# Optimization experiments

Measured on AMD Instinct MI355X. Metric: run time of the kernel, lower is better.

The kernel has to match this reference:

```python
import jax, jax.numpy as jnp
import numpy as np

H = 8        # num_heads
KNN = 16     # k nearest neighbors
D = 256      # input_dim
LN_EPS = 1e-5


def _make_params(key, D):
    ks = jax.random.split(key, 10)
    def lin(k, din, dout):
        k1, k2 = jax.random.split(k)
        lim = 1.0 / np.sqrt(din)
        W = jax.random.uniform(k1, (din, dout), jnp.float32, -lim, lim)
        b = jax.random.uniform(k2, (dout,), jnp.float32, -lim, lim)
        return W, b
    Wq, bq = lin(ks[0], D, D)
    Wk, bk = lin(ks[1], D, D)
    Wv, bv = lin(ks[2], D, D)
    Wo1, bo1 = lin(ks[3], D, D)
    ln_g = jnp.ones((D,), jnp.float32)
    ln_b = jnp.zeros((D,), jnp.float32)
    Wo2, bo2 = lin(ks[4], D, D)
    return dict(Wq=Wq, bq=bq, Wk=Wk, bk=bk, Wv=Wv, bv=bv,
                Wo1=Wo1, bo1=bo1, ln_g=ln_g, ln_b=ln_b, Wo2=Wo2, bo2=bo2)


def setup_inputs() -> dict:
    key = jax.random.key(0)
    k1, k2, k3, k4, k5 = jax.random.split(key, 5)
    B, N, M = 2, 2048, 4096
    inp = {
        "src": jax.random.normal(k1, (B, N, 3), jnp.float32),
        "tgt": jax.random.normal(k2, (B, M, 3), jnp.float32),
        "src_fea": jax.random.normal(k3, (B, N, D), jnp.float32),
        "tgt_fea": jax.random.normal(k4, (B, M, D), jnp.float32),
    }
    inp.update(_make_params(k5, D))
    return inp


def _cdist(x, y):
    # Euclidean distance [B,N,M], matching torch.cdist(p=2)
    x2 = jnp.sum(x * x, axis=-1, keepdims=True)          # [B,N,1]
    y2 = jnp.sum(y * y, axis=-1, keepdims=True)          # [B,M,1]
    sq = x2 + jnp.swapaxes(y2, -1, -2) - 2.0 * jnp.einsum('bnc,bmc->bnm', x, y)
    return jnp.sqrt(jnp.maximum(sq, 0.0))


def _layernorm(x, g, b):
    mu = jnp.mean(x, axis=-1, keepdims=True)
    var = jnp.mean((x - mu) ** 2, axis=-1, keepdims=True)
    return (x - mu) * jax.lax.rsqrt(var + LN_EPS) * g + b


def reference(src, tgt, src_fea, tgt_fea, Wq, bq, Wk, bk, Wv, bv,
              Wo1, bo1, ln_g, ln_b, Wo2, bo2):
    B, N, Dm = src_fea.shape
    M = tgt.shape[1]
    dk = Dm // H
    scale = dk ** (-0.5)

    # kNN mask: distances [B,N,M], topk smallest -> boolean mask
    dist = _cdist(src, tgt)
    _, knn_idx = jax.lax.top_k(-dist, KNN)               # [B,N,KNN]
    bi = jnp.arange(B)[:, None, None]
    ni = jnp.arange(N)[None, :, None]
    mask = jnp.zeros((B, N, M), bool).at[bi, ni, knn_idx].set(True)

    # projections -> [B,H,*,dk]
    Q = (src_fea @ Wq + bq).reshape(B, N, H, dk).transpose(0, 2, 1, 3)
    K = (tgt_fea @ Wk + bk).reshape(B, M, H, dk).transpose(0, 2, 1, 3)
    V = (tgt_fea @ Wv + bv).reshape(B, M, H, dk).transpose(0, 2, 1, 3)

    scores = jnp.einsum('bhnd,bhmd->bhnm', Q, K) * scale
    scores = jnp.where(mask[:, None], scores, -jnp.inf)
    attn = jax.nn.softmax(scores, axis=-1)               # [B,H,N,M]

    out = jnp.einsum('bhnm,bhmd->bhnd', attn, V)
    out = out.transpose(0, 2, 1, 3).reshape(B, N, Dm)

    x = out + src_fea
    h = jax.nn.relu(_layernorm(x @ Wo1 + bo1, ln_g, ln_b))
    updated = h @ Wo2 + bo2

    avg_attn = jnp.mean(attn, axis=1)                    # [B,N,M]
    return updated, avg_attn
```

## Files before the change

### kernel.cpp

```cpp
#include <hip/hip_runtime.h>
#include <math.h>

#define BB 2
#define NN 2048
#define MM 4096
#define DD 256
#define HH 8
#define DK 32
#define KNN 16

typedef __attribute__((ext_vector_type(8))) short short8;
typedef __attribute__((ext_vector_type(4))) short short4v;
typedef __attribute__((ext_vector_type(4))) float f32x4;
typedef unsigned long long u64;
typedef unsigned short u16;

static __device__ __forceinline__ u16 f2bf(float f) {
    union { float f; unsigned u; } v; v.f = f;
    unsigned r = v.u + 0x7FFF + ((v.u >> 16) & 1);
    return (u16)(r >> 16);
}
static __device__ __forceinline__ float bf2f(u16 u) {
    union { unsigned u; float f; } v; v.u = ((unsigned)u) << 16;
    return v.f;
}

__global__ __launch_bounds__(256)
void wtrans(const float* W0, const float* W1, const float* W2, const float* W3, const float* W4,
            u16* O0, u16* O1, u16* O2, u16* O3, u16* O4)
{
    __shared__ float tile[64][65];
    const int bid = blockIdx.x;
    const int m = bid >> 4, tl = bid & 15;
    const int tr = (tl >> 2) * 64, tc = (tl & 3) * 64;
    const float* W = m == 0 ? W0 : m == 1 ? W1 : m == 2 ? W2 : m == 3 ? W3 : W4;
    u16*        O = m == 0 ? O0 : m == 1 ? O1 : m == 2 ? O2 : m == 3 ? O3 : O4;
    const int c = threadIdx.x & 63, r4 = threadIdx.x >> 6;
    #pragma unroll
    for (int i = 0; i < 16; ++i) {
        const int r = (r4 << 4) + i;
        tile[r][c] = W[(size_t)(tr + r) * 256 + tc + c];
    }
    __syncthreads();
    #pragma unroll
    for (int i = 0; i < 16; ++i) {
        const int cc = (r4 << 4) + i;
        O[(size_t)(tc + cc) * 256 + tr + c] = f2bf(tile[c][cc]);
    }
}

static __device__ __forceinline__ void gemm64_body(
    const float* __restrict__ A, size_t row0, const u16* __restrict__ WT, int col0,
    u16* As, u16* Bs, int t, f32x4 acc[2][2])
{
    const int lane = t & 63, w = t >> 6;
    const int wr = (w >> 1) * 32, wc = (w & 1) * 32;
    for (int k0 = 0; k0 < 256; k0 += 64) {
        #pragma unroll
        for (int e = 0; e < 2; ++e) {
            const int flat = t + (e << 8);
            const int r = flat >> 3, kc = (flat & 7) << 3;
            const int off = ((r << 7) + (kc << 1)) ^ ((r & 7) << 4);
            const float* ap = A + (row0 + r) * 256 + k0 + kc;
            float4 a0 = *(const float4*)ap;
            float4 a1 = *(const float4*)(ap + 4);
            short8 s;
            s[0] = (short)f2bf(a0.x); s[1] = (short)f2bf(a0.y);
            s[2] = (short)f2bf(a0.z); s[3] = (short)f2bf(a0.w);
            s[4] = (short)f2bf(a1.x); s[5] = (short)f2bf(a1.y);
            s[6] = (short)f2bf(a1.z); s[7] = (short)f2bf(a1.w);
            *(short8*)((char*)As + off) = s;
            *(short8*)((char*)Bs + off) = *(const short8*)(WT + (size_t)(col0 + r) * 256 + k0 + kc);
        }
        __syncthreads();
        #pragma unroll
        for (int kk = 0; kk < 64; kk += 32) {
            const int kbo = (kk + ((lane >> 4) << 3)) << 1;
            short8 af[2], bfr[2];
            #pragma unroll
            for (int i = 0; i < 2; ++i) {
                const int ra = wr + (i << 4) + (lane & 15);
                af[i]  = *(const short8*)((const char*)As + (((ra << 7) + kbo) ^ ((ra & 7) << 4)));
                const int rb = wc + (i << 4) + (lane & 15);
                bfr[i] = *(const short8*)((const char*)Bs + (((rb << 7) + kbo) ^ ((rb & 7) << 4)));
            }
            #pragma unroll
            for (int mi = 0; mi < 2; ++mi)
                #pragma unroll
                for (int ni = 0; ni < 2; ++ni)
                    acc[mi][ni] = __builtin_amdgcn_mfma_f32_16x16x32_bf16(af[mi], bfr[ni], acc[mi][ni], 0, 0, 0);
        }
        __syncthreads();
    }
}

__global__ __launch_bounds__(256, 4)
void mega_kernel(const float* __restrict__ src, const float* __restrict__ tgt,
                 int* __restrict__ knn_idx,
                 const float* __restrict__ tgt_fea, const float* __restrict__ src_fea,
                 const u16* __restrict__ WTq, const u16* __restrict__ WTkv,
                 const float* __restrict__ bq, const float* __restrict__ bk,
                 const float* __restrict__ bv,
                 float* __restrict__ Qb, u16* __restrict__ Kbf, u16* __restrict__ Vbf,
                 float* __restrict__ avg)
{
    __shared__ u16 As[64 * 64];
    __shared__ u16 Bs[64 * 64];
    const int bid = blockIdx.x;
    const int t = threadIdx.x;
    const int lane = t & 63;
    const int lid = bid / 11;
    const int role = bid % 11;

    if (role < 4) {
        const int kb = lid * 4 + role;
        const int bn = (kb << 2) + (t >> 6);
        const int b = bn >> 11;
        const float* sp = src + (size_t)bn * 3;
        const float px = sp[0], py = sp[1], pz = sp[2];
        const float x2 = px * px + py * py + pz * pz;
        const float* tb = tgt + (size_t)b * MM * 3;
        unsigned key[64];
        #pragma unroll
        for (int j = 0; j < 64; ++j) {
            const int m = (j << 6) + lane;
            const float tx = tb[m * 3 + 0], ty = tb[m * 3 + 1], tz = tb[m * 3 + 2];
            const float y2 = tx * tx + ty * ty + tz * tz;
            const float dt = px * tx + py * ty + pz * tz;
            float d = (x2 + y2) - 2.0f * dt;
            d = d > 0.f ? d : 0.f;
            const unsigned q20 = (unsigned)fminf(d * 32768.0f, 1048575.0f);
            key[j] = (q20 << 12) | (unsigned)m;
        }
        unsigned last1 = 0;
        unsigned mykey = 0xFFFFFFFFu;
        for (int sel = 0; sel < 20; ++sel) {
            unsigned c0 = ~0u, c1 = ~0u, c2 = ~0u, c3 = ~0u;
            #pragma unroll
            for (int j = 0; j < 64; j += 4) {
                const unsigned u0 = key[j + 0] - last1; c0 = u0 < c0 ? u0 : c0;
                const unsigned u1 = key[j + 1] - last1; c1 = u1 < c1 ? u1 : c1;
                const unsigned u2 = key[j + 2] - last1; c2 = u2 < c2 ? u2 : c2;
                const unsigned u3 = key[j + 3] - last1; c3 = u3 < c3 ? u3 : c3;
            }
            unsigned best = c0 < c1 ? c0 : c1;
            const unsigned bst2 = c2 < c3 ? c2 : c3;
            best = best < bst2 ? best : bst2;
            #pragma unroll
            for (int s = 32; s; s >>= 1) {
                const unsigned o = __shfl_xor(best, s, 64);
                best = o < best ? o : best;
            }
            const unsigned winner = best + last1;
            if (lane == sel) mykey = winner;
            last1 = winner + 1;
        }
        const int midx = (int)(mykey & 0xFFFu);
        u64 ex = ~0ULL;
        if (lane < 20) {
            const float* tp = tb + (size_t)midx * 3;
            const double pxd = px, pyd = py, pzd = pz;
            const double tx = tp[0], ty = tp[1], tz = tp[2];
            const double x2d = pxd * pxd + pyd * pyd + pzd * pzd;
            const double y2d = tx * tx + ty * ty + tz * tz;
            const double dtd = pxd * tx + pyd * ty + pzd * tz;
            double dd = (x2d + y2d) - 2.0 * dtd;
            dd = dd > 0.0 ? dd : 0.0;
            ex = (((u64)__double_as_longlong(dd)) & ~0xFFFULL) | (u64)midx;
        }
        int rank = 0;
        #pragma unroll
        for (int i = 0; i < 20; ++i) {
            const u64 o = __shfl(ex, i, 64);
            rank += (o < ex) ? 1 : 0;
        }
        if (lane < 20 && rank < 16)
            knn_idx[(size_t)bn * KNN + rank] = midx;
        return;
    }

    if (role < 8) {
        const int kvb = lid * 4 + (role - 4);
        const size_t row0 = (size_t)(kvb >> 3) * 64;
        const int col0 = (kvb & 7) * 64;
        f32x4 acc[2][2] = {};
        gemm64_body(tgt_fea, row0, WTkv, col0, As, Bs, t, acc);
        const int w = t >> 6;
        const int wr = (w >> 1) * 32, wc = (w & 1) * 32;
        const bool isv = col0 >= 256;
        u16* ob = isv ? Vbf : Kbf;
        const float* bs = isv ? bv : bk;
        const int cb = (isv ? col0 - 256 : col0) + wc;
        const int cq = lane & 15, rq = (lane >> 4) << 2;
        #pragma unroll
        for (int ni = 0; ni < 2; ++ni) {
            const int c = cb + (ni << 4) + cq;
            const float bval = bs[c];
            #pragma unroll
            for (int mi = 0; mi < 2; ++mi) {
                const size_t r = row0 + wr + (mi << 4) + rq;
                #pragma unroll
                for (int e = 0; e < 4; ++e)
                    ob[(r + e) * 256 + c] = f2bf(acc[mi][ni][e] + bval);
            }
        }
        return;
    }

    if (role == 8) {
        const int qb = lid;
        const size_t row0 = (size_t)(qb >> 2) * 64;
        const int col0 = (qb & 3) * 64;
        f32x4 acc[2][2] = {};
        gemm64_body(src_fea, row0, WTq, col0, As, Bs, t, acc);
        const int w = t >> 6;
        const int wr = (w >> 1) * 32, wc = (w & 1) * 32;
        const int cq = lane & 15, rq = (lane >> 4) << 2;
        #pragma unroll
        for (int ni = 0; ni < 2; ++ni) {
            const int c = col0 + wc + (ni << 4) + cq;
            const float bval = bq[c];
            #pragma unroll
            for (int mi = 0; mi < 2; ++mi) {
                const size_t rbase = (row0 + wr + (mi << 4) + rq) * 256 + c;
                #pragma unroll
                for (int e = 0; e < 4; ++e)
                    Qb[rbase + (size_t)e * 256] = acc[mi][ni][e] + bval;
            }
        }
        return;
    }

    {
        const int zb = lid * 2 + (role - 9);
        f32x4 z = {0.f, 0.f, 0.f, 0.f};
        f32x4* pz = (f32x4*)avg;
        const int base = zb * 256 + t;
        #pragma unroll
        for (int i = 0; i < 32; ++i)
            pz[base + i * 131072] = z;
    }
}

__global__ __launch_bounds__(256)
void attn_kernel(const float* __restrict__ Q, const u16* __restrict__ Kb,
                 const u16* __restrict__ Vb, const int* __restrict__ knn_idx,
                 const float* __restrict__ src_fea,
                 u16* __restrict__ Xb, float* __restrict__ avg_attn)
{
    __shared__ float q_sh[4][256];
    __shared__ float pw_sh[4][8][17];
    __shared__ int   idx_sh[4][16];
    const int t = threadIdx.x;
    const int wid = t >> 6, lane = t & 63;
    const int bn = (blockIdx.x << 2) + wid;
    const int b = bn >> 11;
    const int h = lane >> 3, k2 = lane & 7;

    *(float4*)&q_sh[wid][lane << 2] = *(const float4*)(Q + (size_t)bn * 256 + (lane << 2));
    const int ia = knn_idx[(size_t)bn * KNN + k2];
    const int ib = knn_idx[(size_t)bn * KNN + 8 + k2];
    __syncthreads();

    const u16* Ka = Kb + ((size_t)b * MM + ia) * 256 + h * DK;
    const u16* Kc = Kb + ((size_t)b * MM + ib) * 256 + h * DK;
    const float* qh = &q_sh[wid][h * DK];
    float s0 = 0.f, s1 = 0.f;
    #pragma unroll
    for (int j = 0; j < DK; j += 8) {
        const short8 ka = *(const short8*)(Ka + j);
        const short8 kc = *(const short8*)(Kc + j);
        #pragma unroll
        for (int e = 0; e < 8; ++e) {
            const float qv = qh[j + e];
            s0 = fmaf(qv, bf2f((u16)ka[e]), s0);
            s1 = fmaf(qv, bf2f((u16)kc[e]), s1);
        }
    }
    s0 *= 0.17677669529663688f;
    s1 *= 0.17677669529663688f;

    float m = fmaxf(s0, s1);
    m = fmaxf(m, __shfl_xor(m, 1, 64));
    m = fmaxf(m, __shfl_xor(m, 2, 64));
    m = fmaxf(m, __shfl_xor(m, 4, 64));
    const float e0 = expf(s0 - m), e1 = expf(s1 - m);
    float sum = e0 + e1;
    sum += __shfl_xor(sum, 1, 64);
    sum += __shfl_xor(sum, 2, 64);
    sum += __shfl_xor(sum, 4, 64);
    const float inv = 1.0f / sum;
    const float p0 = e0 * inv, p1 = e1 * inv;

    float a0 = p0, a1 = p1;
    a0 += __shfl_xor(a0, 8, 64);  a1 += __shfl_xor(a1, 8, 64);
    a0 += __shfl_xor(a0, 16, 64); a1 += __shfl_xor(a1, 16, 64);
    a0 += __shfl_xor(a0, 32, 64); a1 += __shfl_xor(a1, 32, 64);
    if (h == 0) {
        avg_attn[(size_t)bn * MM + ia] = a0 * 0.125f;
        avg_attn[(size_t)bn * MM + ib] = a1 * 0.125f;
        idx_sh[wid][k2] = ia;
        idx_sh[wid][8 + k2] = ib;
    }
    pw_sh[wid][h][k2] = p0;
    pw_sh[wid][h][8 + k2] = p1;
    __syncthreads();

    const int d0 = lane << 2;
    const int h2 = lane >> 3;
    float o0 = 0.f, o1 = 0.f, o2 = 0.f, o3 = 0.f;
    #pragma unroll
    for (int k = 0; k < KNN; ++k) {
        const float p = pw_sh[wid][h2][k];
        const int ik = idx_sh[wid][k];
        const short4v v4 = *(const short4v*)(Vb + ((size_t)b * MM + ik) * 256 + d0);
        o0 = fmaf(p, bf2f((u16)v4[0]), o0);
        o1 = fmaf(p, bf2f((u16)v4[1]), o1);
        o2 = fmaf(p, bf2f((u16)v4[2]), o2);
        o3 = fmaf(p, bf2f((u16)v4[3]), o3);
    }
    const float4 sf = *(const float4*)(src_fea + (size_t)bn * 256 + d0);
    short4v xo;
    xo[0] = (short)f2bf(o0 + sf.x);
    xo[1] = (short)f2bf(o1 + sf.y);
    xo[2] = (short)f2bf(o2 + sf.z);
    xo[3] = (short)f2bf(o3 + sf.w);
    *(short4v*)(Xb + (size_t)bn * 256 + d0) = xo;
}

__global__ __launch_bounds__(256)
void gemm_wo1_ln(const u16* __restrict__ A, const u16* __restrict__ WT,
                 const float* __restrict__ bias,
                 const float* __restrict__ g, const float* __restrict__ bvec,
                 u16* __restrict__ outb)
{
    __shared__ u16 As[32 * 64];
    __shared__ u16 Bs[256 * 64];
    const int t = threadIdx.x, lane = t & 63, w = t >> 6;
    const size_t row0 = (size_t)blockIdx.x * 32;
    f32x4 acc[2][4] = {};
    for (int k0 = 0; k0 < 256; k0 += 64) {
        {
            const int r = t >> 3, kc = (t & 7) << 3;
            const int off = ((r << 7) + (kc << 1)) ^ ((r & 7) << 4);
            *(short8*)((char*)As + off) = *(const short8*)(A + (row0 + r) * 256 + k0 + kc);
        }
        #pragma unroll
        for (int e = 0; e < 8; ++e) {
            const int u = t + (e << 8);
            const int r = u >> 3, kc = (u & 7) << 3;
            const int off = ((r << 7) + (kc << 1)) ^ ((r & 7) << 4);
            *(short8*)((char*)Bs + off) = *(const short8*)(WT + (size_t)r * 256 + k0 + kc);
        }
        __syncthreads();
        #pragma unroll
        for (int kk = 0; kk < 64; kk += 32) {
            const int kbo = (kk + ((lane >> 4) << 3)) << 1;
            short8 af[2], bfr[4];
            #pragma unroll
            for (int i = 0; i < 2; ++i) {
                const int ra = (i << 4) + (lane & 15);
                af[i] = *(const short8*)((const char*)As + (((ra << 7) + kbo) ^ ((ra & 7) << 4)));
            }
            #pragma unroll
            for (int i = 0; i < 4; ++i) {
                const int rb = (w << 6) + (i << 4) + (lane & 15);
                bfr[i] = *(const short8*)((const char*)Bs + (((rb << 7) + kbo) ^ ((rb & 7) << 4)));
            }
            #pragma unroll
            for (int mi = 0; mi < 2; ++mi)
                #pragma unroll
                for (int ni = 0; ni < 4; ++ni)
                    acc[mi][ni] = __builtin_amdgcn_mfma_f32_16x16x32_bf16(af[mi], bfr[ni], acc[mi][ni], 0, 0, 0);
        }
        __syncthreads();
    }
    const int cq = lane & 15, rq = (lane >> 4) << 2;
    #pragma unroll
    for (int ni = 0; ni < 4; ++ni) {
        const float bval = bias[(w << 6) + (ni << 4) + cq];
        #pragma unroll
        for (int mi = 0; mi < 2; ++mi)
            #pragma unroll
            for (int e = 0; e < 4; ++e)
                acc[mi][ni][e] += bval;
    }
    float* ws1 = (float*)As;
    float* ws2 = ws1 + 128;
    #pragma unroll
    for (int mi = 0; mi < 2; ++mi)
        #pragma unroll
        for (int e = 0; e < 4; ++e) {
            float s1 = 0.f, s2 = 0.f;
            #pragma unroll
            for (int ni = 0; ni < 4; ++ni) { const float y = acc[mi][ni][e]; s1 += y; s2 += y * y; }
            s1 += __shfl_xor(s1, 1, 64); s2 += __shfl_xor(s2, 1, 64);
            s1 += __shfl_xor(s1, 2, 64); s2 += __shfl_xor(s2, 2, 64);
            s1 += __shfl_xor(s1, 4, 64); s2 += __shfl_xor(s2, 4, 64);
            s1 += __shfl_xor(s1, 8, 64); s2 += __shfl_xor(s2, 8, 64);
            if (cq == 0) {
                const int r = (mi << 4) + rq + e;
                ws1[(w << 5) + r] = s1;
                ws2[(w << 5) + r] = s2;
            }
        }
    __syncthreads();
    float g4[4], b4[4];
    #pragma unroll
    for (int ni = 0; ni < 4; ++ni) {
        const int c = (w << 6) + (ni << 4) + cq;
        g4[ni] = g[c]; b4[ni] = bvec[c];
    }
    #pragma unroll
    for (int mi = 0; mi < 2; ++mi)
        #pragma unroll
        for (int e = 0; e < 4; ++e) {
            const int r = (mi << 4) + rq + e;
            const float s1 = ws1[r] + ws1[32 + r] + ws1[64 + r] + ws1[96 + r];
            const float s2 = ws2[r] + ws2[32 + r] + ws2[64 + r] + ws2[96 + r];
            const float mean = s1 * (1.0f / 256.0f);
            const float var = s2 * (1.0f / 256.0f) - mean * mean;
            const float rstd = 1.0f / sqrtf(var + 1e-5f);
            #pragma unroll
            for (int ni = 0; ni < 4; ++ni) {
                const int c = (w << 6) + (ni << 4) + cq;
                const float y = (acc[mi][ni][e] - mean) * rstd * g4[ni] + b4[ni];
                outb[(row0 + r) * 256 + c] = f2bf(fmaxf(y, 0.0f));
            }
        }
}

__global__ __launch_bounds__(256)
void gemm_wo2(const u16* __restrict__ A, const u16* __restrict__ WT,
              const float* __restrict__ bias, float* __restrict__ outf)
{
    __shared__ u16 As[32 * 64];
    __shared__ u16 Bs[128 * 64];
    const int t = threadIdx.x, lane = t & 63, w = t >> 6;
    const size_t row0 = (size_t)(blockIdx.x >> 1) * 32;
    const int col0 = (blockIdx.x & 1) * 128;
    f32x4 acc[2][2] = {};
    for (int k0 = 0; k0 < 256; k0 += 64) {
        {
            const int r = t >> 3, kc = (t & 7) << 3;
            const int off = ((r << 7) + (kc << 1)) ^ ((r & 7) << 4);
            *(short8*)((char*)As + off) = *(const short8*)(A + (row0 + r) * 256 + k0 + kc);
        }
        #pragma unroll
        for (int e = 0; e < 4; ++e) {
            const int u = t + (e << 8);
            const int r = u >> 3, kc = (u & 7) << 3;
            const int off = ((r << 7) + (kc << 1)) ^ ((r & 7) << 4);
            *(short8*)((char*)Bs + off) = *(const short8*)(WT + (size_t)(col0 + r) * 256 + k0 + kc);
        }
        __syncthreads();
        #pragma unroll
        for (int kk = 0; kk < 64; kk += 32) {
            const int kbo = (kk + ((lane >> 4) << 3)) << 1;
            short8 af[2], bfr[2];
            #pragma unroll
            for (int i = 0; i < 2; ++i) {
                const int ra = (i << 4) + (lane & 15);
                af[i] = *(const short8*)((const char*)As + (((ra << 7) + kbo) ^ ((ra & 7) << 4)));
                const int rb = (w << 5) + (i << 4) + (lane & 15);
                bfr[i] = *(const short8*)((const char*)Bs + (((rb << 7) + kbo) ^ ((rb & 7) << 4)));
            }
            #pragma unroll
            for (int mi = 0; mi < 2; ++mi)
                #pragma unroll
                for (int ni = 0; ni < 2; ++ni)
                    acc[mi][ni] = __builtin_amdgcn_mfma_f32_16x16x32_bf16(af[mi], bfr[ni], acc[mi][ni], 0, 0, 0);
        }
        __syncthreads();
    }
    const int cq = lane & 15, rq = (lane >> 4) << 2;
    #pragma unroll
    for (int ni = 0; ni < 2; ++ni) {
        const int c = col0 + (w << 5) + (ni << 4) + cq;
        const float bval = bias[c];
        #pragma unroll
        for (int mi = 0; mi < 2; ++mi) {
            const size_t rbase = (row0 + (mi << 4) + rq) * 256 + c;
            #pragma unroll
            for (int e = 0; e < 4; ++e)
                outf[rbase + (size_t)e * 256] = acc[mi][ni][e] + bval;
        }
    }
}

extern "C" void kernel_launch(void* const* d_in, const int* in_sizes, int n_in,
                              void* d_out, int out_size, void* d_ws, size_t ws_size,
                              hipStream_t stream) {
    const float* src     = (const float*)d_in[0];
    const float* tgt     = (const float*)d_in[1];
    const float* src_fea = (const float*)d_in[2];
    const float* tgt_fea = (const float*)d_in[3];
    const float* Wq  = (const float*)d_in[4];   const float* bq  = (const float*)d_in[5];
    const float* Wk  = (const float*)d_in[6];   const float* bk  = (const float*)d_in[7];
    const float* Wv  = (const float*)d_in[8];   const float* bv  = (const float*)d_in[9];
    const float* Wo1 = (const float*)d_in[10];  const float* bo1 = (const float*)d_in[11];
    const float* lng = (const float*)d_in[12];  const float* lnb = (const float*)d_in[13];
    const float* Wo2 = (const float*)d_in[14];  const float* bo2 = (const float*)d_in[15];
    (void)in_sizes; (void)n_in; (void)out_size; (void)ws_size;

    float* out     = (float*)d_out;
    float* updated = out;
    float* avg     = out + (size_t)BB * NN * DD;

    char* p = (char*)d_ws;
    u16* WTq  = (u16*)p;   p += 256 * 256 * 2;
    u16* WTk  = (u16*)p;   p += 256 * 256 * 2;
    u16* WTv  = (u16*)p;   p += 256 * 256 * 2;
    u16* WTo1 = (u16*)p;   p += 256 * 256 * 2;
    u16* WTo2 = (u16*)p;   p += 256 * 256 * 2;
    float* Qb = (float*)p; p += (size_t)BB * NN * DD * 4;
    u16* Kbf  = (u16*)p;   p += (size_t)BB * MM * DD * 2;
    u16* Vbf  = (u16*)p;   p += (size_t)BB * MM * DD * 2;
    int* knn  = (int*)p;   p += (size_t)BB * NN * KNN * 4;
    u16* Xbf  = (u16*)p;   p += (size_t)BB * NN * DD * 2;
    u16* Hbf  = (u16*)p;   p += (size_t)BB * NN * DD * 2;

    dim3 blk(256);
    wtrans<<<80, blk, 0, stream>>>(Wq, Wk, Wv, Wo1, Wo2, WTq, WTk, WTv, WTo1, WTo2);
    mega_kernel<<<2816, blk, 0, stream>>>(src, tgt, knn, tgt_fea, src_fea, WTq, WTk,
                                          bq, bk, bv, Qb, Kbf, Vbf, avg);
    attn_kernel<<<BB * NN / 4, blk, 0, stream>>>(Qb, Kbf, Vbf, knn, src_fea, Xbf, avg);
    gemm_wo1_ln<<<BB * NN / 32, blk, 0, stream>>>(Xbf, WTo1, bo1, lng, lnb, Hbf);
    gemm_wo2<<<BB * NN / 16, blk, 0, stream>>>(Hbf, WTo2, bo2, updated);
}
```

Before: 183.7 us.

## Fuse attention, Wo1+LayerNorm and Wo2 GEMMs into a single tail kernel

Replaces the separate attention, Wo1+LN and Wo2 kernels with one kernel per 4 query rows. It keeps the attention output and the LN/ReLU activations in shared memory, padded to a 16-row MFMA tile with zero rows. This removes two launches and the global round trips of the intermediate X and H buffers. In exchange, only 4 of the 16 MFMA rows are useful, and every block streams both full weight matrices directly from global/L2 with no LDS staging. That greatly raises total weight-read traffic.

```diff
diff --git a/kernel.cpp b/kernel.cpp
--- a/kernel.cpp
+++ b/kernel.cpp
@@ -147,8 +147,8 @@
             const unsigned bst2 = c2 < c3 ? c2 : c3;
             best = best < bst2 ? best : bst2;
             #pragma unroll
-            for (int s = 32; s; s >>= 1) {
-                const unsigned o = __shfl_xor(best, s, 64);
+            for (int s2 = 32; s2; s2 >>= 1) {
+                const unsigned o = __shfl_xor(best, s2, 64);
                 best = o < best ? o : best;
             }
             const unsigned winner = best + last1;
@@ -243,28 +243,44 @@
 }
 
 __global__ __launch_bounds__(256)
-void attn_kernel(const float* __restrict__ Q, const u16* __restrict__ Kb,
+void tail_kernel(const float* __restrict__ Q, const u16* __restrict__ Kb,
                  const u16* __restrict__ Vb, const int* __restrict__ knn_idx,
                  const float* __restrict__ src_fea,
-                 u16* __restrict__ Xb, float* __restrict__ avg_attn)
+                 const u16* __restrict__ WTo1, const float* __restrict__ bo1,
+                 const float* __restrict__ lng, const float* __restrict__ lnb,
+                 const u16* __restrict__ WTo2, const float* __restrict__ bo2,
+                 float* __restrict__ updated, float* __restrict__ avg_attn)
 {
     __shared__ float q_sh[4][256];
     __shared__ float pw_sh[4][8][17];
     __shared__ int   idx_sh[4][16];
+    __shared__ u16   Xs[16 * 256];
+    __shared__ u16   Hs[16 * 256];
+    __shared__ float2 red2[4][4];
     const int t = threadIdx.x;
-    const int wid = t >> 6, lane = t & 63;
-    const int bn = (blockIdx.x << 2) + wid;
+    const int w = t >> 6, lane = t & 63;
+    const int r0 = blockIdx.x << 2;
+    const int bn = r0 + w;
     const int b = bn >> 11;
     const int h = lane >> 3, k2 = lane & 7;
 
-    *(float4*)&q_sh[wid][lane << 2] = *(const float4*)(Q + (size_t)bn * 256 + (lane << 2));
+    {
+        unsigned* xz = (unsigned*)Xs;
+        unsigned* hz = (unsigned*)Hs;
+        #pragma unroll
+        for (int i = 0; i < 6; ++i) {
+            xz[512 + t + i * 256] = 0u;
+            hz[512 + t + i * 256] = 0u;
+        }
+    }
+
+    *(float4*)&q_sh[w][lane << 2] = *(const float4*)(Q + (size_t)bn * 256 + (lane << 2));
     const int ia = knn_idx[(size_t)bn * KNN + k2];
     const int ib = knn_idx[(size_t)bn * KNN + 8 + k2];
-    __syncthreads();
 
     const u16* Ka = Kb + ((size_t)b * MM + ia) * 256 + h * DK;
     const u16* Kc = Kb + ((size_t)b * MM + ib) * 256 + h * DK;
-    const float* qh = &q_sh[wid][h * DK];
+    const float* qh = &q_sh[w][h * DK];
     float s0 = 0.f, s1 = 0.f;
     #pragma unroll
     for (int j = 0; j < DK; j += 8) {
@@ -280,11 +296,11 @@
     s0 *= 0.17677669529663688f;
     s1 *= 0.17677669529663688f;
 
-    float m = fmaxf(s0, s1);
-    m = fmaxf(m, __shfl_xor(m, 1, 64));
-    m = fmaxf(m, __shfl_xor(m, 2, 64));
-    m = fmaxf(m, __shfl_xor(m, 4, 64));
-    const float e0 = expf(s0 - m), e1 = expf(s1 - m);
+    float mx = fmaxf(s0, s1);
+    mx = fmaxf(mx, __shfl_xor(mx, 1, 64));
+    mx = fmaxf(mx, __shfl_xor(mx, 2, 64));
+    mx = fmaxf(mx, __shfl_xor(mx, 4, 64));
+    const float e0 = expf(s0 - mx), e1 = expf(s1 - mx);
     float sum = e0 + e1;
     sum += __shfl_xor(sum, 1, 64);
     sum += __shfl_xor(sum, 2, 64);
@@ -299,191 +315,117 @@
     if (h == 0) {
         avg_attn[(size_t)bn * MM + ia] = a0 * 0.125f;
         avg_attn[(size_t)bn * MM + ib] = a1 * 0.125f;
-        idx_sh[wid][k2] = ia;
-        idx_sh[wid][8 + k2] = ib;
-    }
-    pw_sh[wid][h][k2] = p0;
-    pw_sh[wid][h][8 + k2] = p1;
+        idx_sh[w][k2] = ia;
+        idx_sh[w][8 + k2] = ib;
+    }
+    pw_sh[w][h][k2] = p0;
+    pw_sh[w][h][8 + k2] = p1;
+
+    {
+        const int d0 = lane << 2;
+        const int h2 = lane >> 3;
+        float o0 = 0.f, o1 = 0.f, o2 = 0.f, o3 = 0.f;
+        #pragma unroll
+        for (int k = 0; k < KNN; ++k) {
+            const float p = pw_sh[w][h2][k];
+            const int ik = idx_sh[w][k];
+            const short4v v4 = *(const short4v*)(Vb + ((size_t)b * MM + ik) * 256 + d0);
+            o0 = fmaf(p, bf2f((u16)v4[0]), o0);
+            o1 = fmaf(p, bf2f((u16)v4[1]), o1);
+            o2 = fmaf(p, bf2f((u16)v4[2]), o2);
+            o3 = fmaf(p, bf2f((u16)v4[3]), o3);
+        }
+        const float4 sf = *(const float4*)(src_fea + (size_t)bn * 256 + d0);
+        short4v xo;
+        xo[0] = (short)f2bf(o0 + sf.x);
+        xo[1] = (short)f2bf(o1 + sf.y);
+        xo[2] = (short)f2bf(o2 + sf.z);
+        xo[3] = (short)f2bf(o3 + sf.w);
+        const int off = ((w << 9) + (d0 << 1)) ^ ((w & 7) << 4);
+        *(short4v*)((char*)Xs + off) = xo;
+    }
     __syncthreads();
 
-    const int d0 = lane << 2;
-    const int h2 = lane >> 3;
-    float o0 = 0.f, o1 = 0.f, o2 = 0.f, o3 = 0.f;
+    const int cq = lane & 15, ks = lane >> 4;
+    f32x4 acc1[4] = {};
     #pragma unroll
-    for (int k = 0; k < KNN; ++k) {
-        const float p = pw_sh[wid][h2][k];
-        const int ik = idx_sh[wid][k];
-        const short4v v4 = *(const short4v*)(Vb + ((size_t)b * MM + ik) * 256 + d0);
-        o0 = fmaf(p, bf2f((u16)v4[0]), o0);
-        o1 = fmaf(p, bf2f((u16)v4[1]), o1);
-        o2 = fmaf(p, bf2f((u16)v4[2]), o2);
-        o3 = fmaf(p, bf2f((u16)v4[3]), o3);
-    }
-    const float4 sf = *(const float4*)(src_fea + (size_t)bn * 256 + d0);
-    short4v xo;
-    xo[0] = (short)f2bf(o0 + sf.x);
-    xo[1] = (short)f2bf(o1 + sf.y);
-    xo[2] = (short)f2bf(o2 + sf.z);
-    xo[3] = (short)f2bf(o3 + sf.w);
-    *(short4v*)(Xb + (size_t)bn * 256 + d0) = xo;
-}
-
-__global__ __launch_bounds__(256)
-void gemm_wo1_ln(const u16* __restrict__ A, const u16* __restrict__ WT,
-                 const float* __restrict__ bias,
-                 const float* __restrict__ g, const float* __restrict__ bvec,
-                 u16* __restrict__ outb)
-{
-    __shared__ u16 As[32 * 64];
-    __shared__ u16 Bs[256 * 64];
-    const int t = threadIdx.x, lane = t & 63, w = t >> 6;
-    const size_t row0 = (size_t)blockIdx.x * 32;
-    f32x4 acc[2][4] = {};
-    for (int k0 = 0; k0 < 256; k0 += 64) {
-        {
-            const int r = t >> 3, kc = (t & 7) << 3;
-            const int off = ((r << 7) + (kc << 1)) ^ ((r & 7) << 4);
-            *(short8*)((char*)As + off) = *(const short8*)(A + (row0 + r) * 256 + k0 + kc);
-        }
-        #pragma unroll
-        for (int e = 0; e < 8; ++e) {
-            const int u = t + (e << 8);
-            const int r = u >> 3, kc = (u & 7) << 3;
-            const int off = ((r << 7) + (kc << 1)) ^ ((r & 7) << 4);
-            *(short8*)((char*)Bs + off) = *(const short8*)(WT + (size_t)r * 256 + k0 + kc);
-        }
-        __syncthreads();
-        #pragma unroll
-        for (int kk = 0; kk < 64; kk += 32) {
-            const int kbo = (kk + ((lane >> 4) << 3)) << 1;
-            short8 af[2], bfr[4];
-            #pragma unroll
-            for (int i = 0; i < 2; ++i) {
-                const int ra = (i << 4) + (lane & 15);
-                af[i] = *(const short8*)((const char*)As + (((ra << 7) + kbo) ^ ((ra & 7) << 4)));
-            }
-            #pragma unroll
-            for (int i = 0; i < 4; ++i) {
-                const int rb = (w << 6) + (i << 4) + (lane & 15);
-                bfr[i] = *(const short8*)((const char*)Bs + (((rb << 7) + kbo) ^ ((rb & 7) << 4)));
-            }
-            #pragma unroll
-            for (int mi = 0; mi < 2; ++mi)
-                #pragma unroll
-                for (int ni = 0; ni < 4; ++ni)
-                    acc[mi][ni] = __builtin_amdgcn_mfma_f32_16x16x32_bf16(af[mi], bfr[ni], acc[mi][ni], 0, 0, 0);
-        }
-        __syncthreads();
-    }
-    const int cq = lane & 15, rq = (lane >> 4) << 2;
+    for (int s = 0; s < 4; ++s) {
+        const int colB = (w << 6) + (s << 4) + cq;
+        const u16* bp = WTo1 + (size_t)colB * 256;
+        #pragma unroll
+        for (int kk = 0; kk < 256; kk += 32) {
+            const int k8 = kk + (ks << 3);
+            const short8 af = *(const short8*)((const char*)Xs + (((cq << 9) + (k8 << 1)) ^ ((cq & 7) << 4)));
+            const short8 bfrg = *(const short8*)(bp + k8);
+            acc1[s] = __builtin_amdgcn_mfma_f32_16x16x32_bf16(af, bfrg, acc1[s], 0, 0, 0);
+        }
+        const float bval = bo1[colB];
+        #pragma unroll
+        for (int e = 0; e < 4; ++e) acc1[s][e] += bval;
+    }
+    {
+        #pragma unroll
+        for (int e = 0; e < 4; ++e) {
+            float v = acc1[0][e] + acc1[1][e] + acc1[2][e] + acc1[3][e];
+            float vv = acc1[0][e]*acc1[0][e] + acc1[1][e]*acc1[1][e]
+                     + acc1[2][e]*acc1[2][e] + acc1[3][e]*acc1[3][e];
+            v += __shfl_xor(v, 1, 64); vv += __shfl_xor(vv, 1, 64);
+            v += __shfl_xor(v, 2, 64); vv += __shfl_xor(vv, 2, 64);
+            v += __shfl_xor(v, 4, 64); vv += __shfl_xor(vv, 4, 64);
+            v += __shfl_xor(v, 8, 64); vv += __shfl_xor(vv, 8, 64);
+            if (ks == 0 && cq == 0) {
+                float2 pr; pr.x = v; pr.y = vv;
+                red2[w][e] = pr;
+            }
+        }
+    }
+    __syncthreads();
+    if (ks == 0) {
+        float g4[4], b4[4];
+        #pragma unroll
+        for (int s = 0; s < 4; ++s) {
+            const int colB = (w << 6) + (s << 4) + cq;
+            g4[s] = lng[colB]; b4[s] = lnb[colB];
+        }
+        #pragma unroll
+        for (int e = 0; e < 4; ++e) {
+            float S1 = 0.f, S2 = 0.f;
+            #pragma unroll
+            for (int w2 = 0; w2 < 4; ++w2) {
+                const float2 pr = red2[w2][e];
+                S1 += pr.x; S2 += pr.y;
+            }
+            const float mean = S1 * (1.0f / 256.0f);
+            const float var = S2 * (1.0f / 256.0f) - mean * mean;
+            const float rstd = 1.0f / sqrtf(var + 1e-5f);
+            #pragma unroll
+            for (int s = 0; s < 4; ++s) {
+                const int colB = (w << 6) + (s << 4) + cq;
+                const float y = (acc1[s][e] - mean) * rstd * g4[s] + b4[s];
+                const int off = ((e << 9) + (colB << 1)) ^ ((e & 7) << 4);
+                *(u16*)((char*)Hs + off) = f2bf(fmaxf(y, 0.0f));
+            }
+        }
+    }
+    __syncthreads();
+
     #pragma unroll
-    for (int ni = 0; ni < 4; ++ni) {
-        const float bval = bias[(w << 6) + (ni << 4) + cq];
-        #pragma unroll
-        for (int mi = 0; mi < 2; ++mi)
+    for (int s = 0; s < 4; ++s) {
+        const int colB = (w << 6) + (s << 4) + cq;
+        const u16* bp = WTo2 + (size_t)colB * 256;
+        f32x4 acc2 = {};
+        #pragma unroll
+        for (int kk = 0; kk < 256; kk += 32) {
+            const int k8 = kk + (ks << 3);
+            const short8 af = *(const short8*)((const char*)Hs + (((cq << 9) + (k8 << 1)) ^ ((cq & 7) << 4)));
+            const short8 bfrg = *(const short8*)(bp + k8);
+            acc2 = __builtin_amdgcn_mfma_f32_16x16x32_bf16(af, bfrg, acc2, 0, 0, 0);
+        }
+        if (ks == 0) {
+            const float bval = bo2[colB];
             #pragma unroll
             for (int e = 0; e < 4; ++e)
-                acc[mi][ni][e] += bval;
-    }
-    float* ws1 = (float*)As;
-    float* ws2 = ws1 + 128;
-    #pragma unroll
-    for (int mi = 0; mi < 2; ++mi)
-        #pragma unroll
-        for (int e = 0; e < 4; ++e) {
-            float s1 = 0.f, s2 = 0.f;
-            #pragma unroll
-            for (int ni = 0; ni < 4; ++ni) { const float y = acc[mi][ni][e]; s1 += y; s2 += y * y; }
-            s1 += __shfl_xor(s1, 1, 64); s2 += __shfl_xor(s2, 1, 64);
-            s1 += __shfl_xor(s1, 2, 64); s2 += __shfl_xor(s2, 2, 64);
-            s1 += __shfl_xor(s1, 4, 64); s2 += __shfl_xor(s2, 4, 64);
-            s1 += __shfl_xor(s1, 8, 64); s2 += __shfl_xor(s2, 8, 64);
-            if (cq == 0) {
-                const int r = (mi << 4) + rq + e;
-                ws1[(w << 5) + r] = s1;
-                ws2[(w << 5) + r] = s2;
-            }
-        }
-    __syncthreads();
-    float g4[4], b4[4];
-    #pragma unroll
-    for (int ni = 0; ni < 4; ++ni) {
-        const int c = (w << 6) + (ni << 4) + cq;
-        g4[ni] = g[c]; b4[ni] = bvec[c];
-    }
-    #pragma unroll
-    for (int mi = 0; mi < 2; ++mi)
-        #pragma unroll
-        for (int e = 0; e < 4; ++e) {
-            const int r = (mi << 4) + rq + e;
-            const float s1 = ws1[r] + ws1[32 + r] + ws1[64 + r] + ws1[96 + r];
-            const float s2 = ws2[r] + ws2[32 + r] + ws2[64 + r] + ws2[96 + r];
-            const float mean = s1 * (1.0f / 256.0f);
-            const float var = s2 * (1.0f / 256.0f) - mean * mean;
-            const float rstd = 1.0f / sqrtf(var + 1e-5f);
-            #pragma unroll
-            for (int ni = 0; ni < 4; ++ni) {
-                const int c = (w << 6) + (ni << 4) + cq;
-                const float y = (acc[mi][ni][e] - mean) * rstd * g4[ni] + b4[ni];
-                outb[(row0 + r) * 256 + c] = f2bf(fmaxf(y, 0.0f));
-            }
-        }
-}
-
-__global__ __launch_bounds__(256)
-void gemm_wo2(const u16* __restrict__ A, const u16* __restrict__ WT,
-              const float* __restrict__ bias, float* __restrict__ outf)
-{
-    __shared__ u16 As[32 * 64];
-    __shared__ u16 Bs[128 * 64];
-    const int t = threadIdx.x, lane = t & 63, w = t >> 6;
-    const size_t row0 = (size_t)(blockIdx.x >> 1) * 32;
-    const int col0 = (blockIdx.x & 1) * 128;
-    f32x4 acc[2][2] = {};
-    for (int k0 = 0; k0 < 256; k0 += 64) {
-        {
-            const int r = t >> 3, kc = (t & 7) << 3;
-            const int off = ((r << 7) + (kc << 1)) ^ ((r & 7) << 4);
-            *(short8*)((char*)As + off) = *(const short8*)(A + (row0 + r) * 256 + k0 + kc);
-        }
-        #pragma unroll
-        for (int e = 0; e < 4; ++e) {
-            const int u = t + (e << 8);
-            const int r = u >> 3, kc = (u & 7) << 3;
-            const int off = ((r << 7) + (kc << 1)) ^ ((r & 7) << 4);
-            *(short8*)((char*)Bs + off) = *(const short8*)(WT + (size_t)(col0 + r) * 256 + k0 + kc);
-        }
-        __syncthreads();
-        #pragma unroll
-        for (int kk = 0; kk < 64; kk += 32) {
-            const int kbo = (kk + ((lane >> 4) << 3)) << 1;
-            short8 af[2], bfr[2];
-            #pragma unroll
-            for (int i = 0; i < 2; ++i) {
-                const int ra = (i << 4) + (lane & 15);
-                af[i] = *(const short8*)((const char*)As + (((ra << 7) + kbo) ^ ((ra & 7) << 4)));
-                const int rb = (w << 5) + (i << 4) + (lane & 15);
-                bfr[i] = *(const short8*)((const char*)Bs + (((rb << 7) + kbo) ^ ((rb & 7) << 4)));
-            }
-            #pragma unroll
-            for (int mi = 0; mi < 2; ++mi)
-                #pragma unroll
-                for (int ni = 0; ni < 2; ++ni)
-                    acc[mi][ni] = __builtin_amdgcn_mfma_f32_16x16x32_bf16(af[mi], bfr[ni], acc[mi][ni], 0, 0, 0);
-        }
-        __syncthreads();
-    }
-    const int cq = lane & 15, rq = (lane >> 4) << 2;
-    #pragma unroll
-    for (int ni = 0; ni < 2; ++ni) {
-        const int c = col0 + (w << 5) + (ni << 4) + cq;
-        const float bval = bias[c];
-        #pragma unroll
-        for (int mi = 0; mi < 2; ++mi) {
-            const size_t rbase = (row0 + (mi << 4) + rq) * 256 + c;
-            #pragma unroll
-            for (int e = 0; e < 4; ++e)
-                outf[rbase + (size_t)e * 256] = acc[mi][ni][e] + bval;
+                updated[(size_t)(r0 + e) * 256 + colB] = acc2[e] + bval;
         }
     }
 }
@@ -517,14 +459,12 @@
     u16* Kbf  = (u16*)p;   p += (size_t)BB * MM * DD * 2;
     u16* Vbf  = (u16*)p;   p += (size_t)BB * MM * DD * 2;
     int* knn  = (int*)p;   p += (size_t)BB * NN * KNN * 4;
-    u16* Xbf  = (u16*)p;   p += (size_t)BB * NN * DD * 2;
-    u16* Hbf  = (u16*)p;   p += (size_t)BB * NN * DD * 2;
 
     dim3 blk(256);
     wtrans<<<80, blk, 0, stream>>>(Wq, Wk, Wv, Wo1, Wo2, WTq, WTk, WTv, WTo1, WTo2);
     mega_kernel<<<2816, blk, 0, stream>>>(src, tgt, knn, tgt_fea, src_fea, WTq, WTk,
                                           bq, bk, bv, Qb, Kbf, Vbf, avg);
-    attn_kernel<<<BB * NN / 4, blk, 0, stream>>>(Qb, Kbf, Vbf, knn, src_fea, Xbf, avg);
-    gemm_wo1_ln<<<BB * NN / 32, blk, 0, stream>>>(Xbf, WTo1, bo1, lng, lnb, Hbf);
-    gemm_wo2<<<BB * NN / 16, blk, 0, stream>>>(Hbf, WTo2, bo2, updated);
-}
+    tail_kernel<<<1024, blk, 0, stream>>>(Qb, Kbf, Vbf, knn, src_fea,
+                                          WTo1, bo1, lng, lnb, WTo2, bo2,
+                                          updated, avg);
+}
```

Result: slower. 196.2 us (+6.8%).
